# Kernel optimization log

Hardware: AMD Instinct MI355X
Metric: run time of the kernel (lower is better)

## Reference

```python
import jax, jax.numpy as jnp
import numpy as np

N_NODES = 50000
N_EDGES = 800000
D = 64  # in_feat == hidden_channels


def _param(key, shape, fan_in):
    return jax.random.normal(key, shape, dtype=jnp.float32) / np.sqrt(fan_in)


def setup_inputs() -> dict:
    key = jax.random.key(0)
    ks = jax.random.split(key, 32)
    inp = {
        "x": jax.random.normal(ks[0], (N_NODES, D), dtype=jnp.float32),
        "edge_index": jax.random.randint(ks[1], (2, N_EDGES), 0, N_NODES, dtype=jnp.int64),
    }
    i = 2
    for l in (1, 2, 3):
        inp[f"W1_{l}"] = _param(ks[i + 0], (D, D), D)   # LEConv lin1 (source nodes)
        inp[f"b1_{l}"] = jnp.zeros((D,), jnp.float32)
        inp[f"W2_{l}"] = _param(ks[i + 1], (D, D), D)   # LEConv lin2 (target nodes, no bias)
        inp[f"W3_{l}"] = _param(ks[i + 2], (D, D), D)   # LEConv lin3 (root/self)
        inp[f"b3_{l}"] = jnp.zeros((D,), jnp.float32)
        inp[f"Wl_{l}"] = _param(ks[i + 3], (D, D), D)   # post-conv Linear
        inp[f"bl_{l}"] = jnp.zeros((D,), jnp.float32)
        i += 4
    return inp


def _leconv(x, src, dst, W1, b1, W2, W3, b3):
    # out_i = lin3(x_i) + sum_{j->i} (lin1(x_j) - lin2(x_i))
    a = x @ W1 + b1          # [N, D]
    b = x @ W2               # [N, D]
    msg = a[src] - b[dst]    # [E, D]  gather + elementwise
    agg = jax.ops.segment_sum(msg, dst, num_segments=x.shape[0])  # scatter-add
    return agg + (x @ W3 + b3)


def reference(x, edge_index,
              W1_1, b1_1, W2_1, W3_1, b3_1, Wl_1, bl_1,
              W1_2, b1_2, W2_2, W3_2, b3_2, Wl_2, bl_2,
              W1_3, b1_3, W2_3, W3_3, b3_3, Wl_3, bl_3):
    src, dst = edge_index[0], edge_index[1]
    h = x
    for (W1, b1, W2, W3, b3, Wl, bl) in (
        (W1_1, b1_1, W2_1, W3_1, b3_1, Wl_1, bl_1),
        (W1_2, b1_2, W2_2, W3_2, b3_2, Wl_2, bl_2),
        (W1_3, b1_3, W2_3, W3_3, b3_3, Wl_3, bl_3),
    ):
        h = _leconv(h, src, dst, W1, b1, W2, W3, b3)
        h = jax.nn.relu(h @ Wl + bl)
    return h
```

## Files before the change

### kernel.cpp

```cpp
#include <hip/hip_runtime.h>

#define N_NODES 50000
#define N_PAD 50176
#define N_EDGES 800000
#define NCHUNK 128
#define NRANGE 4
#define RNODES 12544
#define CEDGES (N_EDGES / NCHUNK)
#define HIST_NB (NCHUNK * NRANGE)
#define SCAN_NB 782
#define GATB 12500
#define NBLK 782

typedef __attribute__((ext_vector_type(8))) short short8;
typedef __attribute__((ext_vector_type(4))) float f32x4;

struct LPtrs { const float *W1, *W2, *W3, *Wl, *b1, *b3, *bl; };
struct AllPtrs { LPtrs l[3]; };

__device__ inline unsigned short f2b(float f) {
    union { float f; unsigned u; } c; c.f = f;
    return (unsigned short)((c.u + 0x7FFFu + ((c.u >> 16) & 1u)) >> 16);
}
__device__ inline float b2f(unsigned short h) {
    union { unsigned u; float f; } c; c.u = ((unsigned)h) << 16;
    return c.f;
}

__global__ __launch_bounds__(256) void histcast_kernel(
    const int* __restrict__ dst, unsigned char* __restrict__ hist_part,
    AllPtrs ap, unsigned short* __restrict__ Wp, float* __restrict__ rows,
    const float* __restrict__ x, unsigned short* __restrict__ h0)
{
    __shared__ unsigned int h[5248];
    const int t = threadIdx.x;
    if (blockIdx.x < HIST_NB) {
        const int chunk = blockIdx.x >> 2;
        const int range = blockIdx.x & 3;
        const int nbase = range * RNODES;
        for (int i = t; i < RNODES / 4; i += 256) h[i] = 0u;
        __syncthreads();
        const int* dp = dst + chunk * CEDGES;
        for (int i = t; i < CEDGES; i += 256) {
            int d = dp[i] - nbase;
            if ((unsigned)d < (unsigned)RNODES)
                atomicAdd(&h[d >> 2], 1u << ((d & 3) * 8));
        }
        __syncthreads();
        unsigned int* out = (unsigned int*)(hist_part + (long)chunk * N_PAD + nbase);
        for (int i = t; i < RNODES / 4; i += 256) out[i] = h[i];
    } else if (blockIdx.x < HIST_NB + 36) {
        float* sW = (float*)h;
        float* sL = (float*)h + 64 * 65;
        const int wi = blockIdx.x - HIST_NB;
        const int layer = wi / 12;
        const int ct = wi % 12;
        LPtrs L = ap.l[layer];
        const float* Wm = (ct < 4) ? L.W1 : (ct < 8) ? L.W2 : L.W3;
        const int colb = (ct & 3) * 16;
        for (int i = t; i < 64 * 64; i += 256) sW[(i >> 6) * 65 + (i & 63)] = Wm[i];
        for (int i = t; i < 64 * 16; i += 256) {
            int q = i >> 4, c = i & 15;
            sL[q * 17 + c] = L.Wl[q * 64 + colb + c];
        }
        __syncthreads();
        for (int local = t; local < 1024; local += 256) {
            int j = local & 7, lane = (local >> 3) & 63, s = local >> 9;
            int k = s * 32 + (lane >> 4) * 8 + j;
            int c = lane & 15;
            float acc = 0.f;
            #pragma unroll 8
            for (int q = 0; q < 64; ++q) acc += sW[k * 65 + q] * sL[q * 17 + c];
            Wp[layer * 12288 + ct * 1024 + local] = f2b(acc);
        }
        if (ct == 0 && t < 64) {
            int col = t;
            float r1 = 0.f, r3 = 0.f;
            for (int q = 0; q < 64; ++q) {
                float wl = L.Wl[q * 64 + col];
                r1 += L.b1[q] * wl;
                r3 += L.b3[q] * wl;
            }
            rows[layer * 128 + col] = r1;
            rows[layer * 128 + 64 + col] = r3 + L.bl[col];
        }
    } else {
        const int cb = blockIdx.x - HIST_NB - 36;
        const long base = (long)cb * 4096 + t * 16;
        if (base < (long)N_NODES * 64) {
            const float4* xp = (const float4*)(x + base);
            float4 f0 = xp[0], f1 = xp[1], f2 = xp[2], f3 = xp[3];
            short8 r0, r1v;
            r0[0] = (short)f2b(f0.x); r0[1] = (short)f2b(f0.y);
            r0[2] = (short)f2b(f0.z); r0[3] = (short)f2b(f0.w);
            r0[4] = (short)f2b(f1.x); r0[5] = (short)f2b(f1.y);
            r0[6] = (short)f2b(f1.z); r0[7] = (short)f2b(f1.w);
            r1v[0] = (short)f2b(f2.x); r1v[1] = (short)f2b(f2.y);
            r1v[2] = (short)f2b(f2.z); r1v[3] = (short)f2b(f2.w);
            r1v[4] = (short)f2b(f3.x); r1v[5] = (short)f2b(f3.y);
            r1v[6] = (short)f2b(f3.z); r1v[7] = (short)f2b(f3.w);
            *(short8*)(h0 + base) = r0;
            *(short8*)(h0 + base + 8) = r1v;
        }
    }
}

__global__ __launch_bounds__(256) void scanA2_kernel(unsigned char* __restrict__ hist_part,
                                                     int* __restrict__ off,
                                                     int* __restrict__ deg,
                                                     int* __restrict__ bsum) {
    __shared__ int part[4][64];
    const int t = threadIdx.x;
    const int ln = t & 63;
    const int cg = t >> 6;
    const int node = blockIdx.x * 64 + ln;
    unsigned char* col = hist_part + node;
    unsigned char v[32];
    int s = 0;
    #pragma unroll
    for (int k = 0; k < 32; ++k) {
        v[k] = col[(long)(cg * 32 + k) * N_PAD];
        s += v[k];
    }
    part[cg][ln] = s;
    __syncthreads();
    int run = 0, tot = 0;
    #pragma unroll
    for (int g = 0; g < 4; ++g) {
        int p = part[g][ln];
        if (g < cg) run += p;
        tot += p;
    }
    #pragma unroll
    for (int k = 0; k < 32; ++k) {
        col[(long)(cg * 32 + k) * N_PAD] = (unsigned char)run;
        run += v[k];
    }
    if (cg == 0) {
        deg[node] = tot;
        int xv = tot;
        #pragma unroll
        for (int d = 1; d < 64; d <<= 1) {
            int u = __shfl_up(xv, d, 64);
            if (ln >= d) xv += u;
        }
        off[node] = xv - tot;
        if (ln == 63) bsum[blockIdx.x] = xv;
    }
}

__device__ __forceinline__ void gemmw_body(int blk, int t,
    const unsigned short* __restrict__ hbf, const unsigned short* __restrict__ Wp,
    const int* __restrict__ deg, const float* __restrict__ rows,
    unsigned short* __restrict__ wbf, int n)
{
    const int lane = t & 63;
    const int quad = lane >> 4, lm = lane & 15;
    const int row_base = blk * 64 + (t >> 6) * 16;

    int arow = min(row_base + lm, n - 1);
    const unsigned short* hrow = hbf + (long)arow * 64;
    short8 a0 = *(const short8*)(hrow + quad * 8);
    short8 a1 = *(const short8*)(hrow + 32 + quad * 8);

    const short8* wp = (const short8*)Wp;
    f32x4 acc[8];
    #pragma unroll
    for (int ct = 0; ct < 8; ++ct) {
        int tile = ct + 4;
        f32x4 z = {0.f, 0.f, 0.f, 0.f};
        short8 w0 = wp[(tile * 2 + 0) * 64 + lane];
        short8 w1 = wp[(tile * 2 + 1) * 64 + lane];
        z = __builtin_amdgcn_mfma_f32_16x16x32_bf16(a0, w0, z, 0, 0, 0);
        z = __builtin_amdgcn_mfma_f32_16x16x32_bf16(a1, w1, z, 0, 0, 0);
        acc[ct] = z;
    }

    const int g0 = row_base + quad * 4;
    float dg[4];
    #pragma unroll
    for (int r = 0; r < 4; ++r) dg[r] = (float)deg[min(g0 + r, n - 1)];

    #pragma unroll
    for (int ct = 0; ct < 4; ++ct) {
        int col = ct * 16 + lm;
        float r1 = rows[col];
        float r3 = rows[64 + col];
        #pragma unroll
        for (int r = 0; r < 4; ++r) {
            int g = g0 + r;
            if (g < n) {
                float wv = acc[4 + ct][r] - dg[r] * (acc[ct][r] - r1) + r3;
                wbf[(long)g * 64 + col] = f2b(wv);
            }
        }
    }
}

__global__ __launch_bounds__(256) void fillw_kernel(
    const int* __restrict__ src, const int* __restrict__ dst,
    const int* __restrict__ off, const int* __restrict__ bsum,
    int* __restrict__ boff, const unsigned char* __restrict__ hist_part,
    int* __restrict__ csr,
    const unsigned short* __restrict__ h0, const unsigned short* __restrict__ Wp,
    const int* __restrict__ deg, const float* __restrict__ rows,
    unsigned short* __restrict__ wbf)
{
    __shared__ int cur[RNODES];
    __shared__ int sb[1024];
    if (blockIdx.x >= HIST_NB) {
        gemmw_body(blockIdx.x - HIST_NB, threadIdx.x, h0, Wp, deg, rows,
                   wbf, N_NODES);
        return;
    }
    const int t = threadIdx.x;

    const int i0 = t * 4;
    int a0 = (i0 + 0 < SCAN_NB) ? bsum[i0 + 0] : 0;
    int a1 = (i0 + 1 < SCAN_NB) ? bsum[i0 + 1] : 0;
    int a2 = (i0 + 2 < SCAN_NB) ? bsum[i0 + 2] : 0;
    int a3 = (i0 + 3 < SCAN_NB) ? bsum[i0 + 3] : 0;
    int s = a0 + a1 + a2 + a3;
    cur[t] = s;
    __syncthreads();
    #pragma unroll
    for (int d = 1; d < 256; d <<= 1) {
        int u = (t >= d) ? cur[t - d] : 0;
        __syncthreads();
        cur[t] += u;
        __syncthreads();
    }
    int excl = cur[t] - s;
    sb[i0 + 0] = excl;
    sb[i0 + 1] = excl + a0;
    sb[i0 + 2] = excl + a0 + a1;
    sb[i0 + 3] = excl + a0 + a1 + a2;
    __syncthreads();
    if (blockIdx.x == 0)
        for (int i = t; i < SCAN_NB; i += 256) boff[i] = sb[i];

    const int chunk = blockIdx.x >> 2;
    const int range = blockIdx.x & 3;
    const int nbase = range * RNODES;
    const unsigned char* bp = hist_part + (long)chunk * N_PAD + nbase;
    const int* op = off + nbase;
    const int lim = min(RNODES, N_NODES - nbase);
    for (int i = t; i < lim; i += 256)
        cur[i] = op[i] + sb[(nbase + i) >> 6] + (int)bp[i];
    __syncthreads();
    const int* dp = dst + chunk * CEDGES;
    const int* sp = src + chunk * CEDGES;
    for (int i = t; i < CEDGES; i += 256) {
        int d = dp[i] - nbase;
        if ((unsigned)d < (unsigned)RNODES) {
            int pos = atomicAdd(&cur[d], 1);
            csr[pos] = sp[i];
        }
    }
}

__global__ __launch_bounds__(256) void gatherw_kernel(
    const int* __restrict__ off, const int* __restrict__ boff,
    const int* __restrict__ degv, const int* __restrict__ csr,
    const unsigned short* __restrict__ hbf, unsigned short* __restrict__ Sbf,
    const unsigned short* __restrict__ Wp, const float* __restrict__ rows,
    unsigned short* __restrict__ wbf)
{
    if (blockIdx.x >= GATB) {
        gemmw_body(blockIdx.x - GATB, threadIdx.x, hbf, Wp, degv, rows,
                   wbf, N_NODES);
        return;
    }
    int node = blockIdx.x * 4 + (threadIdx.x >> 6);
    int lane = threadIdx.x & 63;
    const int g = lane >> 4;
    const int f = (lane & 15) * 4;
    int beg = off[node] + boff[node >> 6];
    int end = beg + degv[node];
    float ax = 0.f, ay = 0.f, az = 0.f, aw = 0.f;
    int j = beg;
    for (; j + 16 <= end; j += 16) {
        int s0 = csr[j + g], s1 = csr[j + 4 + g];
        int s2 = csr[j + 8 + g], s3 = csr[j + 12 + g];
        ushort4 v0 = *(const ushort4*)(hbf + (long)s0 * 64 + f);
        ushort4 v1 = *(const ushort4*)(hbf + (long)s1 * 64 + f);
        ushort4 v2 = *(const ushort4*)(hbf + (long)s2 * 64 + f);
        ushort4 v3 = *(const ushort4*)(hbf + (long)s3 * 64 + f);
        ax += b2f(v0.x) + b2f(v1.x) + b2f(v2.x) + b2f(v3.x);
        ay += b2f(v0.y) + b2f(v1.y) + b2f(v2.y) + b2f(v3.y);
        az += b2f(v0.z) + b2f(v1.z) + b2f(v2.z) + b2f(v3.z);
        aw += b2f(v0.w) + b2f(v1.w) + b2f(v2.w) + b2f(v3.w);
    }
    for (; j + 8 <= end; j += 8) {
        int s0 = csr[j + g], s1 = csr[j + 4 + g];
        ushort4 v0 = *(const ushort4*)(hbf + (long)s0 * 64 + f);
        ushort4 v1 = *(const ushort4*)(hbf + (long)s1 * 64 + f);
        ax += b2f(v0.x) + b2f(v1.x);
        ay += b2f(v0.y) + b2f(v1.y);
        az += b2f(v0.z) + b2f(v1.z);
        aw += b2f(v0.w) + b2f(v1.w);
    }
    for (; j < end; j += 4) {
        int jj = j + g;
        if (jj < end) {
            int s0 = csr[jj];
            ushort4 v0 = *(const ushort4*)(hbf + (long)s0 * 64 + f);
            ax += b2f(v0.x); ay += b2f(v0.y); az += b2f(v0.z); aw += b2f(v0.w);
        }
    }
    #pragma unroll
    for (int m = 16; m < 64; m <<= 1) {
        ax += __shfl_xor(ax, m, 64);
        ay += __shfl_xor(ay, m, 64);
        az += __shfl_xor(az, m, 64);
        aw += __shfl_xor(aw, m, 64);
    }
    if (g == 0) {
        ushort4 o;
        o.x = f2b(ax); o.y = f2b(ay); o.z = f2b(az); o.w = f2b(aw);
        *(ushort4*)(Sbf + (long)node * 64 + f) = o;
    }
}

__global__ __launch_bounds__(256) void out_kernel(
    const unsigned short* __restrict__ Sbf, const unsigned short* __restrict__ wbf,
    const unsigned short* __restrict__ Wp,
    unsigned short* __restrict__ hout, float* __restrict__ fout, int last, int n)
{
    const int t = threadIdx.x;
    const int lane = t & 63;
    const int quad = lane >> 4, lm = lane & 15;
    const int row_base = blockIdx.x * 64 + (t >> 6) * 16;

    int arow = min(row_base + lm, n - 1);
    const unsigned short* srow = Sbf + (long)arow * 64;
    short8 a0 = *(const short8*)(srow + quad * 8);
    short8 a1 = *(const short8*)(srow + 32 + quad * 8);

    const short8* wp = (const short8*)Wp;
    f32x4 acc[4];
    #pragma unroll
    for (int ct = 0; ct < 4; ++ct) {
        f32x4 z = {0.f, 0.f, 0.f, 0.f};
        short8 w0 = wp[(ct * 2 + 0) * 64 + lane];
        short8 w1 = wp[(ct * 2 + 1) * 64 + lane];
        z = __builtin_amdgcn_mfma_f32_16x16x32_bf16(a0, w0, z, 0, 0, 0);
        z = __builtin_amdgcn_mfma_f32_16x16x32_bf16(a1, w1, z, 0, 0, 0);
        acc[ct] = z;
    }

    const int g0 = row_base + quad * 4;
    #pragma unroll
    for (int ct = 0; ct < 4; ++ct) {
        int col = ct * 16 + lm;
        #pragma unroll
        for (int r = 0; r < 4; ++r) {
            int g = g0 + r;
            if (g < n) {
                float val = acc[ct][r] + b2f(wbf[(long)g * 64 + col]);
                val = fmaxf(val, 0.f);
                if (last) fout[(long)g * 64 + col] = val;
                else      hout[(long)g * 64 + col] = f2b(val);
            }
        }
    }
}

extern "C" void kernel_launch(void* const* d_in, const int* in_sizes, int n_in,
                              void* d_out, int out_size, void* d_ws, size_t ws_size,
                              hipStream_t stream) {
    const float* x  = (const float*)d_in[0];
    const int*   ei = (const int*)d_in[1];
    const int*   src = ei;
    const int*   dst = ei + N_EDGES;

    char* wsb = (char*)d_ws;
    unsigned char*  hist_part = (unsigned char*)(wsb);
    unsigned short* h0   = (unsigned short*)(wsb + 6500000);
    unsigned short* h1   = (unsigned short*)(wsb + 12900000);
    unsigned short* Sbf  = (unsigned short*)(wsb + 19300000);
    unsigned short* wbf  = (unsigned short*)(wsb + 25700000);
    unsigned short* Wp   = (unsigned short*)(wsb + 32100000);
    float*          rows = (float*)(wsb + 32200000);
    int* deg  = (int*)(wsb + 32300000);
    int* off  = (int*)(wsb + 32600000);
    int* bsum = (int*)(wsb + 32900000);
    int* boff = (int*)(wsb + 32950000);
    int* csr  = (int*)(wsb + 33000000);

    AllPtrs ap;
    for (int l = 0; l < 3; ++l) {
        int base = 2 + l * 7;
        ap.l[l].W1 = (const float*)d_in[base + 0];
        ap.l[l].b1 = (const float*)d_in[base + 1];
        ap.l[l].W2 = (const float*)d_in[base + 2];
        ap.l[l].W3 = (const float*)d_in[base + 3];
        ap.l[l].b3 = (const float*)d_in[base + 4];
        ap.l[l].Wl = (const float*)d_in[base + 5];
        ap.l[l].bl = (const float*)d_in[base + 6];
    }

    histcast_kernel<<<HIST_NB + 36 + 782, 256, 0, stream>>>(
        dst, hist_part, ap, Wp, rows, x, h0);
    scanA2_kernel<<<SCAN_NB, 256, 0, stream>>>(hist_part, off, deg, bsum);
    fillw_kernel<<<HIST_NB + NBLK, 256, 0, stream>>>(
        src, dst, off, bsum, boff, hist_part, csr,
        h0, Wp, deg, rows, wbf);

    gatherw_kernel<<<GATB, 256, 0, stream>>>(
        off, boff, deg, csr, h0, Sbf, Wp, rows, wbf);
    out_kernel<<<NBLK, 256, 0, stream>>>(Sbf, wbf, Wp, h1, nullptr, 0, N_NODES);

    gatherw_kernel<<<GATB + NBLK, 256, 0, stream>>>(
        off, boff, deg, csr, h1, Sbf, Wp + 12288, rows + 128, wbf);
    out_kernel<<<NBLK, 256, 0, stream>>>(Sbf, wbf, Wp + 12288, h0, nullptr, 0, N_NODES);

    gatherw_kernel<<<GATB + NBLK, 256, 0, stream>>>(
        off, boff, deg, csr, h0, Sbf, Wp + 24576, rows + 256, wbf);
    out_kernel<<<NBLK, 256, 0, stream>>>(Sbf, wbf, Wp + 24576, nullptr,
                                         (float*)d_out, 1, N_NODES);
}
```

Baseline: 306.4 us.

## Split node features into two 32-column planes and gather per plane

Stores the bf16 node features and aggregated sums as two planes of 32 columns each, so each gather pass reads 64-byte rows from a half-size working set that fits cache better. The gather launches twice as many blocks, one set per plane, with 8 edge groups per wavefront instead of 4. It also precomputes a packed (offset, degree) array so each node needs one load instead of three. Gemm-side blocks now run first in the grid. The cost is reading the CSR indices twice per layer and doing more, smaller gather blocks.

```diff
diff --git a/kernel.cpp b/kernel.cpp
--- a/kernel.cpp
+++ b/kernel.cpp
@@ -11,6 +11,7 @@
 #define SCAN_NB 782
 #define GATB 12500
 #define NBLK 782
+#define PLANE ((long)N_PAD * 32)
 
 typedef __attribute__((ext_vector_type(8))) short short8;
 typedef __attribute__((ext_vector_type(4))) float f32x4;
@@ -88,6 +89,8 @@
         const int cb = blockIdx.x - HIST_NB - 36;
         const long base = (long)cb * 4096 + t * 16;
         if (base < (long)N_NODES * 64) {
+            const int row = (int)(base >> 6);
+            const int e0 = (int)(base & 63);
             const float4* xp = (const float4*)(x + base);
             float4 f0 = xp[0], f1 = xp[1], f2 = xp[2], f3 = xp[3];
             short8 r0, r1v;
@@ -99,8 +102,9 @@
             r1v[2] = (short)f2b(f2.z); r1v[3] = (short)f2b(f2.w);
             r1v[4] = (short)f2b(f3.x); r1v[5] = (short)f2b(f3.y);
             r1v[6] = (short)f2b(f3.z); r1v[7] = (short)f2b(f3.w);
-            *(short8*)(h0 + base) = r0;
-            *(short8*)(h0 + base + 8) = r1v;
+            unsigned short* dp2 = h0 + (e0 >> 5) * PLANE + (long)row * 32 + (e0 & 31);
+            *(short8*)dp2 = r0;
+            *(short8*)(dp2 + 8) = r1v;
         }
     }
 }
@@ -150,7 +154,7 @@
 }
 
 __device__ __forceinline__ void gemmw_body(int blk, int t,
-    const unsigned short* __restrict__ hbf, const unsigned short* __restrict__ Wp,
+    const unsigned short* __restrict__ hpl, const unsigned short* __restrict__ Wp,
     const int* __restrict__ deg, const float* __restrict__ rows,
     unsigned short* __restrict__ wbf, int n)
 {
@@ -159,9 +163,8 @@
     const int row_base = blk * 64 + (t >> 6) * 16;
 
     int arow = min(row_base + lm, n - 1);
-    const unsigned short* hrow = hbf + (long)arow * 64;
-    short8 a0 = *(const short8*)(hrow + quad * 8);
-    short8 a1 = *(const short8*)(hrow + 32 + quad * 8);
+    short8 a0 = *(const short8*)(hpl + (long)arow * 32 + quad * 8);
+    short8 a1 = *(const short8*)(hpl + PLANE + (long)arow * 32 + quad * 8);
 
     const short8* wp = (const short8*)Wp;
     f32x4 acc[8];
@@ -201,7 +204,7 @@
     const int* __restrict__ src, const int* __restrict__ dst,
     const int* __restrict__ off, const int* __restrict__ bsum,
     int* __restrict__ boff, const unsigned char* __restrict__ hist_part,
-    int* __restrict__ csr,
+    int* __restrict__ csr, int2* __restrict__ rowinfo,
     const unsigned short* __restrict__ h0, const unsigned short* __restrict__ Wp,
     const int* __restrict__ deg, const float* __restrict__ rows,
     unsigned short* __restrict__ wbf)
@@ -245,8 +248,12 @@
     const unsigned char* bp = hist_part + (long)chunk * N_PAD + nbase;
     const int* op = off + nbase;
     const int lim = min(RNODES, N_NODES - nbase);
-    for (int i = t; i < lim; i += 256)
-        cur[i] = op[i] + sb[(nbase + i) >> 6] + (int)bp[i];
+    for (int i = t; i < lim; i += 256) {
+        int c = op[i] + sb[(nbase + i) >> 6] + (int)bp[i];
+        cur[i] = c;
+        if (chunk == 0)
+            rowinfo[nbase + i] = make_int2(c, deg[nbase + i]);
+    }
     __syncthreads();
     const int* dp = dst + chunk * CEDGES;
     const int* sp = src + chunk * CEDGES;
@@ -260,56 +267,41 @@
 }
 
 __global__ __launch_bounds__(256) void gatherw_kernel(
-    const int* __restrict__ off, const int* __restrict__ boff,
-    const int* __restrict__ degv, const int* __restrict__ csr,
-    const unsigned short* __restrict__ hbf, unsigned short* __restrict__ Sbf,
-    const unsigned short* __restrict__ Wp, const float* __restrict__ rows,
-    unsigned short* __restrict__ wbf)
+    const int2* __restrict__ rowinfo, const int* __restrict__ csr,
+    const unsigned short* __restrict__ hpl, unsigned short* __restrict__ Spl,
+    const unsigned short* __restrict__ Wp, const int* __restrict__ degv,
+    const float* __restrict__ rows, unsigned short* __restrict__ wbf, int gw)
 {
-    if (blockIdx.x >= GATB) {
-        gemmw_body(blockIdx.x - GATB, threadIdx.x, hbf, Wp, degv, rows,
-                   wbf, N_NODES);
+    if (blockIdx.x < gw) {
+        gemmw_body(blockIdx.x, threadIdx.x, hpl, Wp, degv, rows, wbf, N_NODES);
         return;
     }
-    int node = blockIdx.x * 4 + (threadIdx.x >> 6);
-    int lane = threadIdx.x & 63;
-    const int g = lane >> 4;
-    const int f = (lane & 15) * 4;
-    int beg = off[node] + boff[node >> 6];
-    int end = beg + degv[node];
+    int pb = blockIdx.x - gw;
+    int plane = 0;
+    if (pb >= GATB) { plane = 1; pb -= GATB; }
+    const int node = pb * 4 + (threadIdx.x >> 6);
+    const int lane = threadIdx.x & 63;
+    const int g = lane >> 3;
+    const int f = (lane & 7) * 4;
+    const unsigned short* hp = hpl + plane * PLANE;
+
+    int2 ri = rowinfo[node];
+    const int beg = ri.x, dgn = ri.y;
     float ax = 0.f, ay = 0.f, az = 0.f, aw = 0.f;
-    int j = beg;
-    for (; j + 16 <= end; j += 16) {
-        int s0 = csr[j + g], s1 = csr[j + 4 + g];
-        int s2 = csr[j + 8 + g], s3 = csr[j + 12 + g];
-        ushort4 v0 = *(const ushort4*)(hbf + (long)s0 * 64 + f);
-        ushort4 v1 = *(const ushort4*)(hbf + (long)s1 * 64 + f);
-        ushort4 v2 = *(const ushort4*)(hbf + (long)s2 * 64 + f);
-        ushort4 v3 = *(const ushort4*)(hbf + (long)s3 * 64 + f);
-        ax += b2f(v0.x) + b2f(v1.x) + b2f(v2.x) + b2f(v3.x);
-        ay += b2f(v0.y) + b2f(v1.y) + b2f(v2.y) + b2f(v3.y);
-        az += b2f(v0.z) + b2f(v1.z) + b2f(v2.z) + b2f(v3.z);
-        aw += b2f(v0.w) + b2f(v1.w) + b2f(v2.w) + b2f(v3.w);
-    }
-    for (; j + 8 <= end; j += 8) {
-        int s0 = csr[j + g], s1 = csr[j + 4 + g];
-        ushort4 v0 = *(const ushort4*)(hbf + (long)s0 * 64 + f);
-        ushort4 v1 = *(const ushort4*)(hbf + (long)s1 * 64 + f);
-        ax += b2f(v0.x) + b2f(v1.x);
-        ay += b2f(v0.y) + b2f(v1.y);
-        az += b2f(v0.z) + b2f(v1.z);
-        aw += b2f(v0.w) + b2f(v1.w);
-    }
-    for (; j < end; j += 4) {
-        int jj = j + g;
-        if (jj < end) {
-            int s0 = csr[jj];
-            ushort4 v0 = *(const ushort4*)(hbf + (long)s0 * 64 + f);
-            ax += b2f(v0.x); ay += b2f(v0.y); az += b2f(v0.z); aw += b2f(v0.w);
-        }
-    }
-    #pragma unroll
-    for (int m = 16; m < 64; m <<= 1) {
+    int j = beg + g;
+    const int nfull = dgn >> 3;
+    for (int k = 0; k < nfull; ++k, j += 8) {
+        int s = csr[j];
+        ushort4 v = *(const ushort4*)(hp + (long)s * 32 + f);
+        ax += b2f(v.x); ay += b2f(v.y); az += b2f(v.z); aw += b2f(v.w);
+    }
+    if (j < beg + dgn) {
+        int s = csr[j];
+        ushort4 v = *(const ushort4*)(hp + (long)s * 32 + f);
+        ax += b2f(v.x); ay += b2f(v.y); az += b2f(v.z); aw += b2f(v.w);
+    }
+    #pragma unroll
+    for (int m = 8; m < 64; m <<= 1) {
         ax += __shfl_xor(ax, m, 64);
         ay += __shfl_xor(ay, m, 64);
         az += __shfl_xor(az, m, 64);
@@ -318,14 +310,14 @@
     if (g == 0) {
         ushort4 o;
         o.x = f2b(ax); o.y = f2b(ay); o.z = f2b(az); o.w = f2b(aw);
-        *(ushort4*)(Sbf + (long)node * 64 + f) = o;
+        *(ushort4*)(Spl + plane * PLANE + (long)node * 32 + f) = o;
     }
 }
 
 __global__ __launch_bounds__(256) void out_kernel(
-    const unsigned short* __restrict__ Sbf, const unsigned short* __restrict__ wbf,
+    const unsigned short* __restrict__ Spl, const unsigned short* __restrict__ wbf,
     const unsigned short* __restrict__ Wp,
-    unsigned short* __restrict__ hout, float* __restrict__ fout, int last, int n)
+    unsigned short* __restrict__ houtpl, float* __restrict__ fout, int last, int n)
 {
     const int t = threadIdx.x;
     const int lane = t & 63;
@@ -333,9 +325,8 @@
     const int row_base = blockIdx.x * 64 + (t >> 6) * 16;
 
     int arow = min(row_base + lm, n - 1);
-    const unsigned short* srow = Sbf + (long)arow * 64;
-    short8 a0 = *(const short8*)(srow + quad * 8);
-    short8 a1 = *(const short8*)(srow + 32 + quad * 8);
+    short8 a0 = *(const short8*)(Spl + (long)arow * 32 + quad * 8);
+    short8 a1 = *(const short8*)(Spl + PLANE + (long)arow * 32 + quad * 8);
 
     const short8* wp = (const short8*)Wp;
     f32x4 acc[4];
@@ -360,7 +351,7 @@
                 float val = acc[ct][r] + b2f(wbf[(long)g * 64 + col]);
                 val = fmaxf(val, 0.f);
                 if (last) fout[(long)g * 64 + col] = val;
-                else      hout[(long)g * 64 + col] = f2b(val);
+                else      houtpl[(col >> 5) * PLANE + (long)g * 32 + (col & 31)] = f2b(val);
             }
         }
     }
@@ -377,16 +368,17 @@
     char* wsb = (char*)d_ws;
     unsigned char*  hist_part = (unsigned char*)(wsb);
     unsigned short* h0   = (unsigned short*)(wsb + 6500000);
-    unsigned short* h1   = (unsigned short*)(wsb + 12900000);
-    unsigned short* Sbf  = (unsigned short*)(wsb + 19300000);
-    unsigned short* wbf  = (unsigned short*)(wsb + 25700000);
-    unsigned short* Wp   = (unsigned short*)(wsb + 32100000);
-    float*          rows = (float*)(wsb + 32200000);
-    int* deg  = (int*)(wsb + 32300000);
-    int* off  = (int*)(wsb + 32600000);
-    int* bsum = (int*)(wsb + 32900000);
-    int* boff = (int*)(wsb + 32950000);
-    int* csr  = (int*)(wsb + 33000000);
+    unsigned short* h1   = (unsigned short*)(wsb + 12950000);
+    unsigned short* Spl  = (unsigned short*)(wsb + 19400000);
+    unsigned short* wbf  = (unsigned short*)(wsb + 25850000);
+    unsigned short* Wp   = (unsigned short*)(wsb + 32300000);
+    float*          rows = (float*)(wsb + 32400000);
+    int*  deg     = (int*)(wsb + 32500000);
+    int*  off     = (int*)(wsb + 32750000);
+    int*  bsum    = (int*)(wsb + 33000000);
+    int*  boff    = (int*)(wsb + 33010000);
+    int2* rowinfo = (int2*)(wsb + 33020000);
+    int*  csr     = (int*)(wsb + 33450000);
 
     AllPtrs ap;
     for (int l = 0; l < 3; ++l) {
@@ -404,19 +396,19 @@
         dst, hist_part, ap, Wp, rows, x, h0);
     scanA2_kernel<<<SCAN_NB, 256, 0, stream>>>(hist_part, off, deg, bsum);
     fillw_kernel<<<HIST_NB + NBLK, 256, 0, stream>>>(
-        src, dst, off, bsum, boff, hist_part, csr,
+        src, dst, off, bsum, boff, hist_part, csr, rowinfo,
         h0, Wp, deg, rows, wbf);
 
-    gatherw_kernel<<<GATB, 256, 0, stream>>>(
-        off, boff, deg, csr, h0, Sbf, Wp, rows, wbf);
-    out_kernel<<<NBLK, 256, 0, stream>>>(Sbf, wbf, Wp, h1, nullptr, 0, N_NODES);
-
-    gatherw_kernel<<<GATB + NBLK, 256, 0, stream>>>(
-        off, boff, deg, csr, h1, Sbf, Wp + 12288, rows + 128, wbf);
-    out_kernel<<<NBLK, 256, 0, stream>>>(Sbf, wbf, Wp + 12288, h0, nullptr, 0, N_NODES);
-
-    gatherw_kernel<<<GATB + NBLK, 256, 0, stream>>>(
-        off, boff, deg, csr, h0, Sbf, Wp + 24576, rows + 256, wbf);
-    out_kernel<<<NBLK, 256, 0, stream>>>(Sbf, wbf, Wp + 24576, nullptr,
+    gatherw_kernel<<<2 * GATB, 256, 0, stream>>>(
+        rowinfo, csr, h0, Spl, Wp, deg, rows, wbf, 0);
+    out_kernel<<<NBLK, 256, 0, stream>>>(Spl, wbf, Wp, h1, nullptr, 0, N_NODES);
+
+    gatherw_kernel<<<NBLK + 2 * GATB, 256, 0, stream>>>(
+        rowinfo, csr, h1, Spl, Wp + 12288, deg, rows + 128, wbf, NBLK);
+    out_kernel<<<NBLK, 256, 0, stream>>>(Spl, wbf, Wp + 12288, h0, nullptr, 0, N_NODES);
+
+    gatherw_kernel<<<NBLK + 2 * GATB, 256, 0, stream>>>(
+        rowinfo, csr, h0, Spl, Wp + 24576, deg, rows + 256, wbf, NBLK);
+    out_kernel<<<NBLK, 256, 0, stream>>>(Spl, wbf, Wp + 24576, nullptr,
                                          (float*)d_out, 1, N_NODES);
 }
```

New measurement: 352.0 us. +14.9%, slower.
